# Optimization experiments

Hardware: AMD Instinct MI355X
Metric: run time of the kernel (lower is better)

Reference implementation:

```python
import jax, jax.numpy as jnp
import numpy as np
from jax import lax

# dims
B, N, K = 8, 1024, 32          # batch, nodes, kNN neighbors
D, H, DH = 256, 8, 32           # node feature width, heads, head dim
TDIM, NB, HID = 16, 32, 128     # time-embed dim, radial basis count, radial MLP hidden
NLAYERS = 3                     # hidden transformer layers
L = NLAYERS + 1                 # + output layer
NS = 128                        # scalar channels sliced into edge attrs
SHD = 9                         # spherical harmonics dim for lmax=2 (1+3+5)
RMAX = 2.0
EIN = NB + TDIM + 2 * NS        # edge-MLP input width


def _sph(u):
    # real spherical harmonics l=0,1,2 with 'component' normalization of unit vec u
    x, y, z = u[..., 0], u[..., 1], u[..., 2]
    l0 = jnp.ones_like(x)[..., None]
    l1 = np.sqrt(3.0) * u
    l2 = jnp.stack([
        np.sqrt(15.0) * x * y,
        np.sqrt(15.0) * y * z,
        0.5 * np.sqrt(5.0) * (3.0 * z * z - 1.0),
        np.sqrt(15.0) * x * z,
        0.5 * np.sqrt(15.0) * (x * x - y * y),
    ], -1)
    return jnp.concatenate([l0, l1, l2], -1)


def _rbf(r):
    # e3nn soft_one_hot_linspace(basis='gaussian', cutoff=False) * sqrt(NB) * 0.95
    centers = jnp.linspace(0.0, RMAX, NB)
    step = RMAX / (NB - 1)
    e = jnp.exp(-((r[..., None] - centers) / step) ** 2) / 1.12
    return e * (NB ** 0.5) * 0.95


def _sus(x):
    # e3nn smooth unit step: exp(-1/x) for x>0 else 0
    return jnp.where(x > 0, jnp.exp(-1.0 / jnp.where(x > 0, x, 1.0)), 0.0)


def setup_inputs() -> dict:
    key = jax.random.key(0)
    ks = jax.random.split(key, 12)
    g = lambda k, shape, fan: (jax.random.normal(k, shape, jnp.float32) / np.sqrt(fan))
    return {
        'x': jax.random.normal(ks[0], (B, N, 3), jnp.float32),
        'y': jax.random.normal(ks[1], (B, N, 3), jnp.float32),
        't': jax.random.uniform(ks[2], (B, TDIM), jnp.float32),
        'W_embed': g(ks[3], (3 + TDIM, D), 3 + TDIM),
        'Wk1': g(ks[4], (L, EIN, HID), EIN),
        'bk1': jnp.zeros((L, HID), jnp.float32),
        'Wk2': g(ks[5], (L, HID, H * DH), HID),
        'Wq': g(ks[6], (L, D, H * DH), D),
        'Wv': g(ks[7], (L, D + SHD, H * DH), D + SHD),
        'Wo': g(ks[8], (NLAYERS, H * DH, D), H * DH),
        'Wo_out': g(ks[9], (H * DH, 3), H * DH),
    }


def _forward(x, y, t, W_embed, Wk1, bk1, Wk2, Wq, Wv, Wo, Wo_out):
    def score(pos, feat, tt):
        # kNN graph: full pairwise distance + top_k (self included, as in source)
        d2 = jnp.sum((pos[:, None, :] - pos[None, :, :]) ** 2, -1)      # [N,N]
        src = lax.top_k(-d2, K)[1]                                       # [N,K], dst = row index
        vec = pos[:, None, :] - pos[src]                                 # pos[dst]-pos[src], [N,K,3]
        r = jnp.linalg.norm(vec, axis=-1)                                # [N,K]
        u = vec / jnp.maximum(r[..., None], 1e-9)
        sh = _sph(u)                                                     # [N,K,SHD]
        cut = 1.4 * _sus(10.0 * (1.0 - r / RMAX))                        # [N,K]
        rbf = _rbf(r) * cut[..., None]                                   # [N,K,NB]
        t_nodes = jnp.broadcast_to(tt, (N, TDIM))
        edge_base = jnp.concatenate([rbf, jnp.broadcast_to(tt, (N, K, TDIM))], -1)
        node = jnp.concatenate([feat, t_nodes], -1) @ W_embed            # [N,D]
        for l in range(L):
            # gather scalar node channels onto edges
            e = jnp.concatenate([edge_base, node[src][..., :NS],
                                 jnp.broadcast_to(node[:, None, :NS], (N, K, NS))], -1)  # [N,K,EIN]
            h = jax.nn.gelu(e @ Wk1[l] + bk1[l])                          # radial MLP
            kf = (h @ Wk2[l]).reshape(N, K, H, DH)
            q = (node @ Wq[l]).reshape(N, H, DH)
            logits = jnp.einsum('nhd,nkhd->nkh', q, kf) / np.sqrt(DH)
            # cutoff-weighted softmax over neighbors (e3nn Transformer style)
            w = cut[..., None] * jnp.exp(logits - logits.max(1, keepdims=True))
            alpha = w / (w.sum(1, keepdims=True) + 1e-9)                  # [N,K,H]
            v = (jnp.concatenate([node[src], sh], -1) @ Wv[l]).reshape(N, K, H, DH)
            agg = jnp.einsum('nkh,nkhd->nhd', alpha, v).reshape(N, H * DH)
            if l < NLAYERS:
                node = node + agg @ Wo[l]                                  # residual
                # scalar activation: gelu on 0e, tanh on 0o, identity on higher l
                node = jnp.concatenate([jax.nn.gelu(node[:, :64]),
                                        jnp.tanh(node[:, 64:NS]),
                                        node[:, NS:]], -1)
            else:
                node = agg @ Wo_out                                        # project to 1x1e
        return node  # [N,3]

    return jax.vmap(score)(x, y, t)


def reference(x, y, t, W_embed, Wk1, bk1, Wk2, Wq, Wv, Wo, Wo_out):
    return _forward(x, y, t, W_embed, Wk1, bk1, Wk2, Wq, Wv, Wo, Wo_out)
```

## Files before the change

kernel.cpp:

```cpp
#include <hip/hip_runtime.h>
#include <math.h>

#define Bb 8
#define Nn 1024
#define Kk 32
#define Dd 256
#define Hh 8
#define DHh 32
#define TDIMt 16
#define NBnb 32
#define HIDh 128
#define NSns 128
#define SHDs 9
#define EINe 304
#define NCOLS 1536

typedef __bf16 bf16_t;
typedef bf16_t bf16x8 __attribute__((ext_vector_type(8)));
typedef float floatx4 __attribute__((ext_vector_type(4)));

#define GLOAD_LDS16(gp, lp) __builtin_amdgcn_global_load_lds( \
    (const __attribute__((address_space(1))) void*)(gp),      \
    (__attribute__((address_space(3))) void*)(lp), 16, 0, 0)

__device__ __forceinline__ float gelu_fast(float x){
  float g = 1.5957691216057308f*(x + 0.044715f*x*x*x);
  return x*__builtin_amdgcn_rcpf(1.0f + __expf(-g));
}
__device__ __forceinline__ float tanh_fast(float x){
  return 1.0f - 2.0f*__builtin_amdgcn_rcpf(1.0f + __expf(2.0f*x));
}

__global__ __launch_bounds__(256) void setup_kernel(
    const float* __restrict__ x, const float* __restrict__ y, const float* __restrict__ t,
    const float* __restrict__ We, const float* __restrict__ Wk1, const float* __restrict__ bk1,
    const float* __restrict__ Wk2, const float* __restrict__ Wq, const float* __restrict__ Wv,
    const float* __restrict__ Wo,
    bf16_t* __restrict__ Wt, bf16_t* __restrict__ Wto, bf16_t* __restrict__ WrbfT,
    float* __restrict__ t_hd, int* __restrict__ src,
    float* __restrict__ node, bf16_t* __restrict__ node_bf){

  __shared__ float s_b[32];
  __shared__ unsigned long long s_knn[4][64];
  const int bid = blockIdx.x, tid = threadIdx.x;

  if (bid < 2048){
    int wave = tid >> 6, lane = tid & 63;
    int bn = bid*4 + wave;
    int b = bn >> 10, n = bn & (Nn-1);
    const float* xb = x + (size_t)b*Nn*3;
    float px = xb[n*3+0], py = xb[n*3+1], pz = xb[n*3+2];
    float d2v[16];
    #pragma unroll
    for (int i=0;i<16;i++){
      int j = i*64 + lane;
      float dx = px - xb[j*3+0];
      float dy = py - xb[j*3+1];
      float dz = pz - xb[j*3+2];
      d2v[i] = dx*dx + dy*dy + dz*dz;
    }

    unsigned lob = 0u, hib = 0x7149F2CAu;
    float T = 1.0f;
    int lc = 0;
    for (int it=0; it<24; ++it){
      lc = 0;
      #pragma unroll
      for (int i=0;i<16;i++) lc += (d2v[i] <= T) ? 1 : 0;
      int c = lc;
      #pragma unroll
      for (int off=32; off>=1; off>>=1) c += __shfl_xor(c, off);
      if (c >= 32 && c <= 64) break;
      if (c < 32) lob = __float_as_uint(T); else hib = __float_as_uint(T);
      float ratio = 44.0f * __builtin_amdgcn_rcpf((float)(c < 1 ? 1 : c));
      float Tn = T * __powf(ratio, 0.6666667f);
      unsigned tb = __float_as_uint(Tn);
      if (tb <= lob || tb >= hib) tb = lob + ((hib - lob) >> 1);
      T = __uint_as_float(tb);
    }

    int pre = lc;
    #pragma unroll
    for (int d=1; d<64; d<<=1){
      int o = __shfl_up(pre, d);
      if (lane >= d) pre += o;
    }
    int wo = pre - lc;

    unsigned long long* sl = s_knn[wave];
    sl[lane] = ~0ull;
    #pragma unroll
    for (int i=0;i<16;i++){
      if (d2v[i] <= T && wo < 64){
        sl[wo] = (((unsigned long long)__float_as_uint(d2v[i])) << 10)
                 | (unsigned)(i*64 + lane);
        wo++;
      }
    }
    __syncthreads();

    unsigned long long key = sl[lane];
    #pragma unroll
    for (int k2=2; k2<=64; k2<<=1){
      #pragma unroll
      for (int j2=k2>>1; j2>=1; j2>>=1){
        unsigned long long pv = __shfl_xor(key, j2);
        bool takeMin = (((lane & j2) == 0) == ((lane & k2) == 0));
        bool pLess = pv < key;
        key = (pLess == takeMin) ? pv : key;
      }
    }
    if (lane < 32) src[(size_t)bn*Kk + lane] = (int)(key & 1023u);
  } else if (bid < 6144){
    int i = bid-2048; int l = i>>10, yy = i&1023;
    int h = yy>>7, c = yy&127;
    if (tid < 32) s_b[tid] = Wk2[(size_t)l*HIDh*Dd + (size_t)c*Dd + h*DHh + tid];
    __syncthreads();
    const int rloc = tid>>3, dg = tid&7;
    const float b0 = s_b[dg*4+0], b1 = s_b[dg*4+1], b2 = s_b[dg*4+2], b3 = s_b[dg*4+3];
    #pragma unroll
    for (int p=0;p<8;p++){
      int ii = p*32 + rloc;
      const float4 v = *(const float4*)(Wq + (size_t)l*Dd*Dd + (size_t)ii*Dd + h*DHh + dg*4);
      float part = v.x*b0 + v.y*b1 + v.z*b2 + v.w*b3;
      part += __shfl_xor(part, 1);
      part += __shfl_xor(part, 2);
      part += __shfl_xor(part, 4);
      if (dg == 0) Wt[((size_t)l*NCOLS + 512 + yy)*Dd + ii] = (bf16_t)part;
    }
  } else if (bid < 8192){
    int i = bid-6144; int l = i>>9, c = i&511, k = tid;
    const float* wk1l = Wk1 + (size_t)l*EINe*HIDh;
    float v;
    if (c < 256)       v = Wv[(size_t)l*265*Dd + (size_t)k*Dd + c];
    else if (c < 384){ int c2 = c-256; v = (k < 128) ? wk1l[(48+k)*HIDh + c2] : 0.0f; }
    else             { int c2 = c-384; v = (k < 128) ? wk1l[(176+k)*HIDh + c2] : 0.0f; }
    Wt[((size_t)l*NCOLS + c)*Dd + k] = (bf16_t)v;
  } else if (bid < 8960){
    int i = bid-8192; int l = i>>8; int c = i&255; int k = tid;
    Wto[((size_t)l*Dd + c)*Dd + k] = (bf16_t)Wo[(size_t)l*Dd*Dd + (size_t)k*Dd + c];
  } else if (bid < 9024){
    int i = bid-8960; int l = i>>4, cg = i&15;
    int c = cg*8 + (tid>>5), k = tid&31;
    WrbfT[((size_t)l*HIDh + c)*NBnb + k] = (bf16_t)Wk1[(size_t)l*EINe*HIDh + (size_t)k*HIDh + c];
  } else if (bid < 9040){
    int i = bid-9024; int pair = i*2 + (tid>>7);
    int l = pair>>3, b = pair&7, c = tid&127;
    const float* wk1l = Wk1 + (size_t)l*EINe*HIDh;
    float a = bk1[l*HIDh + c];
    #pragma unroll
    for (int ii=0;ii<TDIMt;ii++) a += t[b*TDIMt+ii]*wk1l[(32+ii)*HIDh + c];
    t_hd[(l*Bb + b)*HIDh + c] = a;
  } else {
    int bn0 = (bid-9040)*4; int c = tid;
    float w0 = We[0*Dd+c], w1 = We[1*Dd+c], w2 = We[2*Dd+c];
    float wt[TDIMt];
    #pragma unroll
    for (int i=0;i<TDIMt;i++) wt[i] = We[(3+i)*Dd+c];
    #pragma unroll
    for (int u=0;u<4;u++){
      int bn = bn0 + u; int b = bn >> 10;
      float a = y[(size_t)bn*3+0]*w0 + y[(size_t)bn*3+1]*w1 + y[(size_t)bn*3+2]*w2;
      #pragma unroll
      for (int i=0;i<TDIMt;i++) a += t[b*TDIMt+i]*wt[i];
      node[(size_t)bn*Dd + c] = a;
      node_bf[(size_t)bn*Dd + c] = (bf16_t)a;
    }
  }
}

__global__ __launch_bounds__(256) void gemm_proj(const bf16_t* __restrict__ A,
    const bf16_t* __restrict__ Wt_all, float* __restrict__ vproj_f,
    bf16_t* __restrict__ hsrc_bf, float* __restrict__ hdst_f,
    bf16_t* __restrict__ qw_bf, const float* __restrict__ t_hd, int layer){

  __shared__ __align__(16) bf16_t s_A[2][8192];
  __shared__ __align__(16) bf16_t s_B[2][4096];

  const int tid = threadIdx.x;
  const int wave = tid>>6, lane = tid&63;
  const int row16 = lane&15, quad = lane>>4;
  const int bx = blockIdx.x;
  const int brow = ((bx & 7) << 3) + (bx >> 3);
  const int m0 = brow*128;
  const int m_base = m0 + wave*32;
  const int n_base = blockIdx.y*64;
  const bf16_t* Ab = A + (size_t)m0*Dd;
  const bf16_t* Bw = Wt_all + ((size_t)layer*NCOLS + n_base)*Dd;

  const int trow = tid>>3;
  const int tk   = ((tid&7) ^ (trow&7)) << 3;
  const int swz  = (row16&7) << 3;

  floatx4 acc[2][4];
  #pragma unroll
  for (int mi=0;mi<2;mi++)
    #pragma unroll
    for (int ni=0;ni<4;ni++){ floatx4 z = {0.f,0.f,0.f,0.f}; acc[mi][ni] = z; }

  {
    const bf16_t* ga = Ab + (size_t)trow*Dd + tk;
    #pragma unroll
    for (int i=0;i<4;i++) GLOAD_LDS16(ga + (size_t)i*32*Dd, &s_A[0][i*2048 + tid*8]);
    const bf16_t* gb = Bw + (size_t)trow*Dd + tk;
    #pragma unroll
    for (int j=0;j<2;j++) GLOAD_LDS16(gb + (size_t)j*32*Dd, &s_B[0][j*2048 + tid*8]);
  }
  __syncthreads();

  #pragma unroll
  for (int kt=0; kt<4; kt++){
    const int cur = kt&1, nxt = cur^1;
    if (kt < 3){
      const bf16_t* ga = Ab + (size_t)trow*Dd + (kt+1)*64 + tk;
      #pragma unroll
      for (int i=0;i<4;i++) GLOAD_LDS16(ga + (size_t)i*32*Dd, &s_A[nxt][i*2048 + tid*8]);
      const bf16_t* gb = Bw + (size_t)trow*Dd + (kt+1)*64 + tk;
      #pragma unroll
      for (int j=0;j<2;j++) GLOAD_LDS16(gb + (size_t)j*32*Dd, &s_B[nxt][j*2048 + tid*8]);
    }
    #pragma unroll
    for (int ksub=0; ksub<2; ksub++){
      const int ko = (ksub*32 + quad*8) ^ swz;
      bf16x8 a0 = *(const bf16x8*)&s_A[cur][(wave*32      + row16)*64 + ko];
      bf16x8 a1 = *(const bf16x8*)&s_A[cur][(wave*32 + 16 + row16)*64 + ko];
      #pragma unroll
      for (int ni=0;ni<4;ni++){
        bf16x8 b = *(const bf16x8*)&s_B[cur][(ni*16 + row16)*64 + ko];
        acc[0][ni] = __builtin_amdgcn_mfma_f32_16x16x32_bf16(a0, b, acc[0][ni], 0,0,0);
        acc[1][ni] = __builtin_amdgcn_mfma_f32_16x16x32_bf16(a1, b, acc[1][ni], 0,0,0);
      }
    }
    __syncthreads();
  }

  const int by = blockIdx.y;
  const int bb = m_base >> 10;
  #pragma unroll
  for (int mi=0;mi<2;mi++)
    #pragma unroll
    for (int ni=0;ni<4;ni++){
      int col = n_base + ni*16 + row16;
      #pragma unroll
      for (int r=0;r<4;r++){
        int row = m_base + mi*16 + quad*4 + r;
        float v = acc[mi][ni][r];
        if (by < 4)       vproj_f[(size_t)row*256 + col]        = v;
        else if (by < 6)  hsrc_bf[(size_t)row*128 + (col-256)]  = (bf16_t)v;
        else if (by < 8)  hdst_f[(size_t)row*128 + (col-384)]   = v + t_hd[(size_t)(layer*Bb + bb)*HIDh + (col-384)];
        else              qw_bf[(size_t)row*1024 + (col-512)]   = (bf16_t)v;
      }
    }
}

__global__ __launch_bounds__(256) void gemm_upd(
    const bf16_t* __restrict__ agg_bf, const bf16_t* __restrict__ Wto,
    const float* __restrict__ node_in, float* __restrict__ node_out,
    bf16_t* __restrict__ node_bf, int lu, int write_node){

  __shared__ __align__(16) bf16_t s_A[2][8192];
  __shared__ __align__(16) bf16_t s_B[2][4096];

  const int tid = threadIdx.x;
  const int wave = tid>>6, lane = tid&63;
  const int row16 = lane&15, quad = lane>>4;
  const int bx = blockIdx.x;
  const int brow = ((bx & 7) << 3) + (bx >> 3);
  const int m0 = brow*128;
  const int m_base = m0 + wave*32;
  const int n_base = blockIdx.y*64;
  const bf16_t* Ab = agg_bf + (size_t)m0*Dd;
  const bf16_t* Bw = Wto + (size_t)lu*Dd*Dd + (size_t)n_base*Dd;

  const int trow = tid>>3;
  const int tk   = ((tid&7) ^ (trow&7)) << 3;
  const int swz  = (row16&7) << 3;

  floatx4 acc[2][4];
  #pragma unroll
  for (int mi=0;mi<2;mi++)
    #pragma unroll
    for (int ni=0;ni<4;ni++){ floatx4 z = {0.f,0.f,0.f,0.f}; acc[mi][ni] = z; }

  {
    const bf16_t* ga = Ab + (size_t)trow*Dd + tk;
    #pragma unroll
    for (int i=0;i<4;i++) GLOAD_LDS16(ga + (size_t)i*32*Dd, &s_A[0][i*2048 + tid*8]);
    const bf16_t* gb = Bw + (size_t)trow*Dd + tk;
    #pragma unroll
    for (int j=0;j<2;j++) GLOAD_LDS16(gb + (size_t)j*32*Dd, &s_B[0][j*2048 + tid*8]);
  }
  __syncthreads();

  #pragma unroll
  for (int kt=0; kt<4; kt++){
    const int cur = kt&1, nxt = cur^1;
    if (kt < 3){
      const bf16_t* ga = Ab + (size_t)trow*Dd + (kt+1)*64 + tk;
      #pragma unroll
      for (int i=0;i<4;i++) GLOAD_LDS16(ga + (size_t)i*32*Dd, &s_A[nxt][i*2048 + tid*8]);
      const bf16_t* gb = Bw + (size_t)trow*Dd + (kt+1)*64 + tk;
      #pragma unroll
      for (int j=0;j<2;j++) GLOAD_LDS16(gb + (size_t)j*32*Dd, &s_B[nxt][j*2048 + tid*8]);
    }
    #pragma unroll
    for (int ksub=0; ksub<2; ksub++){
      const int ko = (ksub*32 + quad*8) ^ swz;
      bf16x8 a0 = *(const bf16x8*)&s_A[cur][(wave*32      + row16)*64 + ko];
      bf16x8 a1 = *(const bf16x8*)&s_A[cur][(wave*32 + 16 + row16)*64 + ko];
      #pragma unroll
      for (int ni=0;ni<4;ni++){
        bf16x8 b = *(const bf16x8*)&s_B[cur][(ni*16 + row16)*64 + ko];
        acc[0][ni] = __builtin_amdgcn_mfma_f32_16x16x32_bf16(a0, b, acc[0][ni], 0,0,0);
        acc[1][ni] = __builtin_amdgcn_mfma_f32_16x16x32_bf16(a1, b, acc[1][ni], 0,0,0);
      }
    }
    __syncthreads();
  }

  #pragma unroll
  for (int mi=0;mi<2;mi++)
    #pragma unroll
    for (int ni=0;ni<4;ni++){
      int col = n_base + ni*16 + row16;
      #pragma unroll
      for (int r=0;r<4;r++){
        int row = m_base + mi*16 + quad*4 + r;
        float v = acc[mi][ni][r] + node_in[(size_t)row*Dd + col];
        if (col < 64)       v = gelu_fast(v);
        else if (col < 128) v = tanh_fast(v);
        if (write_node) node_out[(size_t)row*Dd + col] = v;
        node_bf[(size_t)row*Dd + col] = (bf16_t)v;
      }
    }
}

__global__ __launch_bounds__(256) void attn_kernel(
    const float* __restrict__ x, const int* __restrict__ src,
    const float* __restrict__ vproj_f, const bf16_t* __restrict__ hsrc_bf,
    const float* __restrict__ hdst_f, const bf16_t* __restrict__ qw_bf,
    const bf16_t* __restrict__ WrbfT,
    const float* __restrict__ Wvg, const float* __restrict__ Woo,
    bf16_t* __restrict__ agg_bf, float* __restrict__ out, int layer){

  __shared__ __align__(16) char smem[23296];
  bf16_t* s_h     = (bf16_t*)(smem);
  float*  s_part  = (float*)(smem);
  float*  s_sh    = (float*)(smem + 17408);
  float*  s_cut   = (float*)(smem + 19968);
  int*    s_srcv  = (int*)  (smem + 20224);
  float*  s_logit = (float*)(smem + 20480);
  float*  s_pool  = (float*)(smem + 22528);
  float*  s_red   = (float*)(smem + 23168);

  const int tid  = threadIdx.x;
  const int bidx = blockIdx.x;
  const int b    = bidx & 7;
  const int bn0  = (b << 10) | ((bidx >> 3) << 1);
  const int wave = tid>>6, lane = tid&63;
  const int side = wave>>1, wv = wave&1;
  const int row16 = lane&15, quad = lane>>4;
  const int bns = bn0 + side;

  bf16x8 qf[4];
  { const bf16_t* qp = qw_bf + (size_t)bns*1024 + row16*HIDh + quad*8;
    #pragma unroll
    for (int ks=0; ks<4; ks++) qf[ks] = *(const bf16x8*)(qp + ks*32); }
  float hdv[4];
  #pragma unroll
  for (int ni=0; ni<4; ni++) hdv[ni] = hdst_f[(size_t)bns*128 + wv*64 + ni*16 + row16];

  const float ax = x[(size_t)bns*3+0], ay = x[(size_t)bns*3+1], az = x[(size_t)bns*3+2];

  const int sE0 = src[(size_t)bns*Kk + row16];
  const int sE1 = src[(size_t)bns*Kk + row16 + 16];

  const int t2 = tid & 127;
  const int e0 = t2>>3, cg = t2&7;
  const int sG0 = src[(size_t)bns*Kk + e0];
  const int sG1 = src[(size_t)bns*Kk + e0 + 16];
  bf16x8 hsv00 = *(const bf16x8*)(hsrc_bf + ((size_t)b*Nn + sG0)*128 + cg*8);
  bf16x8 hsv01 = *(const bf16x8*)(hsrc_bf + ((size_t)b*Nn + sG0)*128 + cg*8 + 64);
  bf16x8 hsv10 = *(const bf16x8*)(hsrc_bf + ((size_t)b*Nn + sG1)*128 + cg*8);
  bf16x8 hsv11 = *(const bf16x8*)(hsrc_bf + ((size_t)b*Nn + sG1)*128 + cg*8 + 64);

  bf16x8 a0f, a1f;
  {
    const float* xj0 = x + ((size_t)b*Nn + sE0)*3;
    const float* xj1 = x + ((size_t)b*Nn + sE1)*3;
    float d0x = ax - xj0[0], d0y = ay - xj0[1], d0z = az - xj0[2];
    float d1x = ax - xj1[0], d1y = ay - xj1[1], d1z = az - xj1[2];
    float rr0 = sqrtf(d0x*d0x + d0y*d0y + d0z*d0z);
    float rr1 = sqrtf(d1x*d1x + d1y*d1y + d1z*d1z);
    float xx0 = 10.0f*(1.0f - rr0*0.5f);
    float xx1 = 10.0f*(1.0f - rr1*0.5f);
    float cu0 = (xx0 > 0.0f) ? 1.4f*__expf(-__builtin_amdgcn_rcpf(xx0)) : 0.0f;
    float cu1 = (xx1 > 0.0f) ? 1.4f*__expf(-__builtin_amdgcn_rcpf(xx1)) : 0.0f;
    float sc0 = 4.798224586623f*cu0;
    float sc1 = 4.798224586623f*cu1;
    float rs0 = fminf(rr0*15.5f, 33.0f);
    float rs1 = fminf(rr1*15.5f, 33.0f);
    float cbase = (float)(quad*8);
    float dd0 = rs0 - cbase, dd1 = rs1 - cbase;
    float e0v = __expf(-dd0*dd0)*sc0;
    float e1v = __expf(-dd1*dd1)*sc1;
    float g0 = __expf(2.0f*dd0 - 1.0f);
    float g1 = __expf(2.0f*dd1 - 1.0f);
    a0f[0] = (bf16_t)e0v; a1f[0] = (bf16_t)e1v;
    #pragma unroll
    for (int j=1;j<8;j++){
      e0v *= g0; e1v *= g1;
      a0f[j] = (bf16_t)e0v; a1f[j] = (bf16_t)e1v;
      g0 *= 0.13533528323661270f; g1 *= 0.13533528323661270f;
    }
  }

  if (tid < 128){
    const int hs = (tid>>6)&1;
    const int k = tid & 31;
    const int hn = bn0 + hs;
    const int j = src[(size_t)hn*Kk + k];
    const float hx = x[(size_t)hn*3+0], hy = x[(size_t)hn*3+1], hz = x[(size_t)hn*3+2];
    const float* xj = x + ((size_t)b*Nn + j)*3;
    float dx = hx - xj[0], dy = hy - xj[1], dz = hz - xj[2];
    float rr = sqrtf(dx*dx + dy*dy + dz*dz);
    if ((tid & 32) == 0){
      s_srcv[hs*32 + k] = j;
      float xx = 10.0f*(1.0f - rr*0.5f);
      s_cut[hs*32 + k] = (xx > 0.0f) ? 1.4f*__expf(-__builtin_amdgcn_rcpf(xx)) : 0.0f;
    } else {
      float inv = __builtin_amdgcn_rcpf(fmaxf(rr, 1e-9f));
      float ux = dx*inv, uy = dy*inv, uz = dz*inv;
      float* sh = s_sh + hs*320 + k*10;
      sh[0] = 1.0f;
      sh[1] = 1.7320508075688772f*ux;
      sh[2] = 1.7320508075688772f*uy;
      sh[3] = 1.7320508075688772f*uz;
      sh[4] = 3.872983346207417f*ux*uy;
      sh[5] = 3.872983346207417f*uy*uz;
      sh[6] = 1.118033988749895f*(3.0f*uz*uz - 1.0f);
      sh[7] = 3.872983346207417f*ux*uz;
      sh[8] = 1.9364916731037085f*(ux*ux - uy*uy);
    }
  }

  floatx4 acc[2][4];
  {
    #pragma unroll
    for (int mi=0;mi<2;mi++)
      #pragma unroll
      for (int ni=0;ni<4;ni++){ floatx4 z = {0.f,0.f,0.f,0.f}; acc[mi][ni] = z; }
    const bf16_t* bp = WrbfT + ((size_t)layer*HIDh + wv*64 + row16)*NBnb + quad*8;
    #pragma unroll
    for (int j=0;j<4;j++){
      bf16x8 bbf = *(const bf16x8*)(bp + (size_t)j*16*NBnb);
      acc[0][j] = __builtin_amdgcn_mfma_f32_16x16x32_bf16(a0f, bbf, acc[0][j], 0,0,0);
      acc[1][j] = __builtin_amdgcn_mfma_f32_16x16x32_bf16(a1f, bbf, acc[1][j], 0,0,0);
    }
  }

  bf16_t* shs = s_h + side*4352;
  *(bf16x8*)(shs + e0*136 + cg*8)            = hsv00;
  *(bf16x8*)(shs + e0*136 + cg*8 + 64)       = hsv01;
  *(bf16x8*)(shs + (e0+16)*136 + cg*8)       = hsv10;
  *(bf16x8*)(shs + (e0+16)*136 + cg*8 + 64)  = hsv11;
  __syncthreads();

  #pragma unroll
  for (int ni=0;ni<4;ni++){
    int c = wv*64 + ni*16 + row16;
    #pragma unroll
    for (int mi=0;mi<2;mi++){
      #pragma unroll
      for (int r=0;r<4;r++){
        int e = mi*16 + quad*4 + r;
        float hs = (float)shs[e*136 + c];
        shs[e*136 + c] = (bf16_t)gelu_fast(acc[mi][ni][r] + hdv[ni] + hs);
      }
    }
  }
  __syncthreads();

  {
    floatx4 la = {0.f,0.f,0.f,0.f};
    #pragma unroll
    for (int ks=0; ks<4; ks++){
      bf16x8 a = *(const bf16x8*)(shs + (wv*16 + row16)*136 + ks*32 + quad*8);
      la = __builtin_amdgcn_mfma_f32_16x16x32_bf16(a, qf[ks], la, 0,0,0);
    }
    if (row16 < Hh){
      #pragma unroll
      for (int r=0;r<4;r++)
        s_logit[side*256 + (wv*16 + quad*4 + r)*8 + row16] = la[r]*0.17677669529663687f;
    }
  }
  __syncthreads();

  {
    const int k = tid & 31;
    const int h = tid >> 5;
    #pragma unroll
    for (int sn=0; sn<2; sn++){
      float lv = s_logit[sn*256 + k*8 + h];
      float m = lv;
      #pragma unroll
      for (int off=16; off>=1; off>>=1) m = fmaxf(m, __shfl_xor(m, off));
      float w = s_cut[sn*32 + k]*__expf(lv - m);
      float ss = w;
      #pragma unroll
      for (int off=16; off>=1; off>>=1) ss += __shfl_xor(ss, off);
      s_logit[sn*256 + k*8 + h] = w*__builtin_amdgcn_rcpf(ss + 1e-9f);
    }
  }
  __syncthreads();

  {
    const int pn = tid>>7, t3 = tid&127, h2 = t3>>4, sg = t3&15;
    if (sg < SHDs){
      float a = 0.0f;
      #pragma unroll
      for (int k2=0;k2<Kk;k2++)
        a += s_logit[pn*256 + k2*8 + h2] * s_sh[pn*320 + k2*10 + sg];
      s_pool[pn*80 + h2*10 + sg] = a;
    }
  }

  {
    const float* rowp[16];
    #pragma unroll
    for (int i=0;i<16;i++){
      int row = __builtin_amdgcn_readfirstlane(s_srcv[side*32 + wv*16 + i]);
      rowp[i] = vproj_f + ((size_t)b*Nn + row)*256;
    }
    const int albase = side*256 + wv*128 + (lane>>3);
    float4 accv = {0.f,0.f,0.f,0.f};
    #pragma unroll
    for (int i=0;i<16;i++){
      const float4 v = *(const float4*)(rowp[i] + (lane<<2));
      float al = s_logit[albase + i*8];
      accv.x += al*v.x; accv.y += al*v.y; accv.z += al*v.z; accv.w += al*v.w;
    }
    *(float4*)(s_part + (side*2 + wv)*256 + (lane<<2)) = accv;
  }
  __syncthreads();

  {
    const int h = tid >> 5;
    const float* wvsh = Wvg + (size_t)layer*265*Dd + 256*Dd;
    float wv9[SHDs];
    #pragma unroll
    for (int sg=0; sg<SHDs; sg++) wv9[sg] = wvsh[sg*Dd + tid];

    float w0=0.f, w1=0.f, w2=0.f;
    if (layer >= 3){ w0 = Woo[tid*3+0]; w1 = Woo[tid*3+1]; w2 = Woo[tid*3+2]; }

    #pragma unroll
    for (int sn=0; sn<2; sn++){
      float a_main = s_part[sn*512 + tid] + s_part[sn*512 + 256 + tid];
      #pragma unroll
      for (int sg=0; sg<SHDs; sg++) a_main += s_pool[sn*80 + h*10 + sg]*wv9[sg];

      if (layer < 3){
        agg_bf[(size_t)(bn0+sn)*Dd + tid] = (bf16_t)a_main;
      } else {
        float p0 = a_main*w0;
        float p1 = a_main*w1;
        float p2 = a_main*w2;
        #pragma unroll
        for (int off=32; off>=1; off>>=1){
          p0 += __shfl_xor(p0, off);
          p1 += __shfl_xor(p1, off);
          p2 += __shfl_xor(p2, off);
        }
        if (lane == 0){
          s_red[sn*12 + wave*3+0] = p0;
          s_red[sn*12 + wave*3+1] = p1;
          s_red[sn*12 + wave*3+2] = p2;
        }
      }
    }
    if (layer >= 3){
      __syncthreads();
      if (tid < 8){
        int sn = tid>>2, j = tid&3;
        if (j < 3)
          out[(size_t)(bn0+sn)*3 + j] = s_red[sn*12 + j] + s_red[sn*12 + 3 + j]
                                      + s_red[sn*12 + 6 + j] + s_red[sn*12 + 9 + j];
      }
    }
  }
}

extern "C" void kernel_launch(void* const* d_in, const int* in_sizes, int n_in,
                              void* d_out, int out_size, void* d_ws, size_t ws_size,
                              hipStream_t stream){
  const float* x   = (const float*)d_in[0];
  const float* y   = (const float*)d_in[1];
  const float* t   = (const float*)d_in[2];
  const float* We  = (const float*)d_in[3];
  const float* Wk1 = (const float*)d_in[4];
  const float* bk1 = (const float*)d_in[5];
  const float* Wk2 = (const float*)d_in[6];
  const float* Wq  = (const float*)d_in[7];
  const float* Wv  = (const float*)d_in[8];
  const float* Wo  = (const float*)d_in[9];
  const float* Woo = (const float*)d_in[10];
  float* out = (float*)d_out;

  char* ws = (char*)d_ws;
  size_t off = 0;
  auto take = [&](size_t bytes)->char*{ char* p = ws + off; off = (off + bytes + 255) & ~(size_t)255; return p; };

  int*    src      = (int*)   take((size_t)Bb*Nn*Kk*4);
  float*  nodeA    = (float*) take((size_t)Bb*Nn*Dd*4);
  float*  nodeB    = (float*) take((size_t)Bb*Nn*Dd*4);
  bf16_t* node_bf  = (bf16_t*)take((size_t)Bb*Nn*Dd*2);
  bf16_t* agg_bf   = (bf16_t*)take((size_t)Bb*Nn*Dd*2);
  float*  vproj_f  = (float*) take((size_t)Bb*Nn*256*4);
  bf16_t* hsrc_bf  = (bf16_t*)take((size_t)Bb*Nn*128*2);
  float*  hdst_f   = (float*) take((size_t)Bb*Nn*128*4);
  bf16_t* qw_bf    = (bf16_t*)take(((size_t)Bb*Nn*1024 + 2048)*2);
  bf16_t* Wt       = (bf16_t*)take((size_t)4*NCOLS*Dd*2);
  bf16_t* Wto      = (bf16_t*)take((size_t)3*Dd*Dd*2);
  bf16_t* WrbfT    = (bf16_t*)take((size_t)4*HIDh*NBnb*2);
  float*  t_hd     = (float*) take((size_t)4*Bb*HIDh*4);

  setup_kernel<<<dim3(11088), 256, 0, stream>>>(x, y, t, We, Wk1, bk1, Wk2, Wq, Wv, Wo,
                                                Wt, Wto, WrbfT, t_hd, src, nodeA, node_bf);

  gemm_proj<<<dim3(64,24), 256, 0, stream>>>(node_bf, Wt, vproj_f, hsrc_bf, hdst_f, qw_bf, t_hd, 0);
  attn_kernel<<<dim3(Bb*Nn/2), 256, 0, stream>>>(x, src, vproj_f, hsrc_bf, hdst_f, qw_bf,
                                                 WrbfT, Wv, Woo, agg_bf, out, 0);
  const float* nin[3]  = {nodeA, nodeB, nodeA};
  float*       nout[3] = {nodeB, nodeA, nodeB};
  for (int l=1; l<4; l++){
    gemm_upd<<<dim3(64,4), 256, 0, stream>>>(agg_bf, Wto, nin[l-1], nout[l-1], node_bf,
                                             l-1, (l < 3) ? 1 : 0);
    gemm_proj<<<dim3(64,24), 256, 0, stream>>>(node_bf, Wt, vproj_f, hsrc_bf, hdst_f, qw_bf, t_hd, l);
    attn_kernel<<<dim3(Bb*Nn/2), 256, 0, stream>>>(x, src, vproj_f, hsrc_bf, hdst_f, qw_bf,
                                                   WrbfT, Wv, Woo, agg_bf, out, l);
  }
}
```

Measured before the change: 391.4 us.

## Process one node per 128-thread attention block instead of two per 256-thread block

Result: no change. 399.0 us (+1.9%).

```diff
diff --git a/kernel.cpp b/kernel.cpp
--- a/kernel.cpp
+++ b/kernel.cpp
@@ -335,7 +335,7 @@
     }
 }
 
-__global__ __launch_bounds__(256) void attn_kernel(
+__global__ __launch_bounds__(128) void attn_kernel(
     const float* __restrict__ x, const int* __restrict__ src,
     const float* __restrict__ vproj_f, const bf16_t* __restrict__ hsrc_bf,
     const float* __restrict__ hdst_f, const bf16_t* __restrict__ qw_bf,
@@ -343,42 +343,38 @@
     const float* __restrict__ Wvg, const float* __restrict__ Woo,
     bf16_t* __restrict__ agg_bf, float* __restrict__ out, int layer){
 
-  __shared__ __align__(16) char smem[23296];
+  __shared__ __align__(16) char smem[11488];
   bf16_t* s_h     = (bf16_t*)(smem);
   float*  s_part  = (float*)(smem);
-  float*  s_sh    = (float*)(smem + 17408);
-  float*  s_cut   = (float*)(smem + 19968);
-  int*    s_srcv  = (int*)  (smem + 20224);
-  float*  s_logit = (float*)(smem + 20480);
-  float*  s_pool  = (float*)(smem + 22528);
-  float*  s_red   = (float*)(smem + 23168);
+  float*  s_sh    = (float*)(smem + 8704);
+  float*  s_cut   = (float*)(smem + 9984);
+  float*  s_logit = (float*)(smem + 10112);
+  float*  s_pool  = (float*)(smem + 11136);
+  float*  s_red   = (float*)(smem + 11456);
 
   const int tid  = threadIdx.x;
   const int bidx = blockIdx.x;
   const int b    = bidx & 7;
-  const int bn0  = (b << 10) | ((bidx >> 3) << 1);
-  const int wave = tid>>6, lane = tid&63;
-  const int side = wave>>1, wv = wave&1;
+  const int bn   = (b << 10) | (bidx >> 3);
+  const int wv   = tid>>6, lane = tid&63;
   const int row16 = lane&15, quad = lane>>4;
-  const int bns = bn0 + side;
 
   bf16x8 qf[4];
-  { const bf16_t* qp = qw_bf + (size_t)bns*1024 + row16*HIDh + quad*8;
+  { const bf16_t* qp = qw_bf + (size_t)bn*1024 + row16*HIDh + quad*8;
     #pragma unroll
     for (int ks=0; ks<4; ks++) qf[ks] = *(const bf16x8*)(qp + ks*32); }
   float hdv[4];
   #pragma unroll
-  for (int ni=0; ni<4; ni++) hdv[ni] = hdst_f[(size_t)bns*128 + wv*64 + ni*16 + row16];
-
-  const float ax = x[(size_t)bns*3+0], ay = x[(size_t)bns*3+1], az = x[(size_t)bns*3+2];
-
-  const int sE0 = src[(size_t)bns*Kk + row16];
-  const int sE1 = src[(size_t)bns*Kk + row16 + 16];
-
-  const int t2 = tid & 127;
-  const int e0 = t2>>3, cg = t2&7;
-  const int sG0 = src[(size_t)bns*Kk + e0];
-  const int sG1 = src[(size_t)bns*Kk + e0 + 16];
+  for (int ni=0; ni<4; ni++) hdv[ni] = hdst_f[(size_t)bn*128 + wv*64 + ni*16 + row16];
+
+  const float ax = x[(size_t)bn*3+0], ay = x[(size_t)bn*3+1], az = x[(size_t)bn*3+2];
+
+  const int sE0 = src[(size_t)bn*Kk + row16];
+  const int sE1 = src[(size_t)bn*Kk + row16 + 16];
+
+  const int e0 = tid>>3, cg = tid&7;
+  const int sG0 = src[(size_t)bn*Kk + e0];
+  const int sG1 = src[(size_t)bn*Kk + e0 + 16];
   bf16x8 hsv00 = *(const bf16x8*)(hsrc_bf + ((size_t)b*Nn + sG0)*128 + cg*8);
   bf16x8 hsv01 = *(const bf16x8*)(hsrc_bf + ((size_t)b*Nn + sG0)*128 + cg*8 + 64);
   bf16x8 hsv10 = *(const bf16x8*)(hsrc_bf + ((size_t)b*Nn + sG1)*128 + cg*8);
@@ -415,23 +411,19 @@
     }
   }
 
-  if (tid < 128){
-    const int hs = (tid>>6)&1;
+  if (tid < 64){
     const int k = tid & 31;
-    const int hn = bn0 + hs;
-    const int j = src[(size_t)hn*Kk + k];
-    const float hx = x[(size_t)hn*3+0], hy = x[(size_t)hn*3+1], hz = x[(size_t)hn*3+2];
+    const int j = src[(size_t)bn*Kk + k];
     const float* xj = x + ((size_t)b*Nn + j)*3;
-    float dx = hx - xj[0], dy = hy - xj[1], dz = hz - xj[2];
+    float dx = ax - xj[0], dy = ay - xj[1], dz = az - xj[2];
     float rr = sqrtf(dx*dx + dy*dy + dz*dz);
-    if ((tid & 32) == 0){
-      s_srcv[hs*32 + k] = j;
+    if (tid < 32){
       float xx = 10.0f*(1.0f - rr*0.5f);
-      s_cut[hs*32 + k] = (xx > 0.0f) ? 1.4f*__expf(-__builtin_amdgcn_rcpf(xx)) : 0.0f;
+      s_cut[k] = (xx > 0.0f) ? 1.4f*__expf(-__builtin_amdgcn_rcpf(xx)) : 0.0f;
     } else {
       float inv = __builtin_amdgcn_rcpf(fmaxf(rr, 1e-9f));
       float ux = dx*inv, uy = dy*inv, uz = dz*inv;
-      float* sh = s_sh + hs*320 + k*10;
+      float* sh = s_sh + k*10;
       sh[0] = 1.0f;
       sh[1] = 1.7320508075688772f*ux;
       sh[2] = 1.7320508075688772f*uy;
@@ -459,11 +451,10 @@
     }
   }
 
-  bf16_t* shs = s_h + side*4352;
-  *(bf16x8*)(shs + e0*136 + cg*8)            = hsv00;
-  *(bf16x8*)(shs + e0*136 + cg*8 + 64)       = hsv01;
-  *(bf16x8*)(shs + (e0+16)*136 + cg*8)       = hsv10;
-  *(bf16x8*)(shs + (e0+16)*136 + cg*8 + 64)  = hsv11;
+  *(bf16x8*)(s_h + e0*136 + cg*8)            = hsv00;
+  *(bf16x8*)(s_h + e0*136 + cg*8 + 64)       = hsv01;
+  *(bf16x8*)(s_h + (e0+16)*136 + cg*8)       = hsv10;
+  *(bf16x8*)(s_h + (e0+16)*136 + cg*8 + 64)  = hsv11;
   __syncthreads();
 
   #pragma unroll
@@ -474,8 +465,8 @@
       #pragma unroll
       for (int r=0;r<4;r++){
         int e = mi*16 + quad*4 + r;
-        float hs = (float)shs[e*136 + c];
-        shs[e*136 + c] = (bf16_t)gelu_fast(acc[mi][ni][r] + hdv[ni] + hs);
+        float hs = (float)s_h[e*136 + c];
+        s_h[e*136 + c] = (bf16_t)gelu_fast(acc[mi][ni][r] + hdv[ni] + hs);
       }
     }
   }
@@ -485,43 +476,44 @@
     floatx4 la = {0.f,0.f,0.f,0.f};
     #pragma unroll
     for (int ks=0; ks<4; ks++){
-      bf16x8 a = *(const bf16x8*)(shs + (wv*16 + row16)*136 + ks*32 + quad*8);
+      bf16x8 a = *(const bf16x8*)(s_h + (wv*16 + row16)*136 + ks*32 + quad*8);
       la = __builtin_amdgcn_mfma_f32_16x16x32_bf16(a, qf[ks], la, 0,0,0);
     }
     if (row16 < Hh){
       #pragma unroll
       for (int r=0;r<4;r++)
-        s_logit[side*256 + (wv*16 + quad*4 + r)*8 + row16] = la[r]*0.17677669529663687f;
+        s_logit[(wv*16 + quad*4 + r)*8 + row16] = la[r]*0.17677669529663687f;
     }
   }
   __syncthreads();
 
   {
     const int k = tid & 31;
-    const int h = tid >> 5;
-    #pragma unroll
-    for (int sn=0; sn<2; sn++){
-      float lv = s_logit[sn*256 + k*8 + h];
+    const int h0 = tid >> 5;
+    #pragma unroll
+    for (int hh=0; hh<2; hh++){
+      const int h = h0 + hh*4;
+      float lv = s_logit[k*8 + h];
       float m = lv;
       #pragma unroll
       for (int off=16; off>=1; off>>=1) m = fmaxf(m, __shfl_xor(m, off));
-      float w = s_cut[sn*32 + k]*__expf(lv - m);
+      float w = s_cut[k]*__expf(lv - m);
       float ss = w;
       #pragma unroll
       for (int off=16; off>=1; off>>=1) ss += __shfl_xor(ss, off);
-      s_logit[sn*256 + k*8 + h] = w*__builtin_amdgcn_rcpf(ss + 1e-9f);
+      s_logit[k*8 + h] = w*__builtin_amdgcn_rcpf(ss + 1e-9f);
     }
   }
   __syncthreads();
 
   {
-    const int pn = tid>>7, t3 = tid&127, h2 = t3>>4, sg = t3&15;
+    const int h2 = tid>>4, sg = tid&15;
     if (sg < SHDs){
       float a = 0.0f;
       #pragma unroll
       for (int k2=0;k2<Kk;k2++)
-        a += s_logit[pn*256 + k2*8 + h2] * s_sh[pn*320 + k2*10 + sg];
-      s_pool[pn*80 + h2*10 + sg] = a;
+        a += s_logit[k2*8 + h2] * s_sh[k2*10 + sg];
+      s_pool[h2*10 + sg] = a;
     }
   }
 
@@ -529,10 +521,10 @@
     const float* rowp[16];
     #pragma unroll
     for (int i=0;i<16;i++){
-      int row = __builtin_amdgcn_readfirstlane(s_srcv[side*32 + wv*16 + i]);
+      int row = __builtin_amdgcn_readfirstlane(src[(size_t)bn*Kk + wv*16 + i]);
       rowp[i] = vproj_f + ((size_t)b*Nn + row)*256;
     }
-    const int albase = side*256 + wv*128 + (lane>>3);
+    const int albase = wv*128 + (lane>>3);
     float4 accv = {0.f,0.f,0.f,0.f};
     #pragma unroll
     for (int i=0;i<16;i++){
@@ -540,53 +532,40 @@
       float al = s_logit[albase + i*8];
       accv.x += al*v.x; accv.y += al*v.y; accv.z += al*v.z; accv.w += al*v.w;
     }
-    *(float4*)(s_part + (side*2 + wv)*256 + (lane<<2)) = accv;
+    *(float4*)(s_part + wv*256 + (lane<<2)) = accv;
   }
   __syncthreads();
 
   {
-    const int h = tid >> 5;
     const float* wvsh = Wvg + (size_t)layer*265*Dd + 256*Dd;
-    float wv9[SHDs];
-    #pragma unroll
-    for (int sg=0; sg<SHDs; sg++) wv9[sg] = wvsh[sg*Dd + tid];
-
-    float w0=0.f, w1=0.f, w2=0.f;
-    if (layer >= 3){ w0 = Woo[tid*3+0]; w1 = Woo[tid*3+1]; w2 = Woo[tid*3+2]; }
-
-    #pragma unroll
-    for (int sn=0; sn<2; sn++){
-      float a_main = s_part[sn*512 + tid] + s_part[sn*512 + 256 + tid];
-      #pragma unroll
-      for (int sg=0; sg<SHDs; sg++) a_main += s_pool[sn*80 + h*10 + sg]*wv9[sg];
+    float p0 = 0.f, p1 = 0.f, p2 = 0.f;
+    #pragma unroll
+    for (int cc=0; cc<2; cc++){
+      const int c = tid + cc*128;
+      const int h = c >> 5;
+      float a_main = s_part[c] + s_part[256 + c];
+      #pragma unroll
+      for (int sg=0; sg<SHDs; sg++) a_main += s_pool[h*10 + sg]*wvsh[sg*Dd + c];
 
       if (layer < 3){
-        agg_bf[(size_t)(bn0+sn)*Dd + tid] = (bf16_t)a_main;
+        agg_bf[(size_t)bn*Dd + c] = (bf16_t)a_main;
       } else {
-        float p0 = a_main*w0;
-        float p1 = a_main*w1;
-        float p2 = a_main*w2;
-        #pragma unroll
-        for (int off=32; off>=1; off>>=1){
-          p0 += __shfl_xor(p0, off);
-          p1 += __shfl_xor(p1, off);
-          p2 += __shfl_xor(p2, off);
-        }
-        if (lane == 0){
-          s_red[sn*12 + wave*3+0] = p0;
-          s_red[sn*12 + wave*3+1] = p1;
-          s_red[sn*12 + wave*3+2] = p2;
-        }
+        p0 += a_main*Woo[c*3+0];
+        p1 += a_main*Woo[c*3+1];
+        p2 += a_main*Woo[c*3+2];
       }
     }
     if (layer >= 3){
+      #pragma unroll
+      for (int off=32; off>=1; off>>=1){
+        p0 += __shfl_xor(p0, off);
+        p1 += __shfl_xor(p1, off);
+        p2 += __shfl_xor(p2, off);
+      }
+      if (lane == 0){ s_red[wv*3+0]=p0; s_red[wv*3+1]=p1; s_red[wv*3+2]=p2; }
       __syncthreads();
-      if (tid < 8){
-        int sn = tid>>2, j = tid&3;
-        if (j < 3)
-          out[(size_t)(bn0+sn)*3 + j] = s_red[sn*12 + j] + s_red[sn*12 + 3 + j]
-                                      + s_red[sn*12 + 6 + j] + s_red[sn*12 + 9 + j];
-      }
+      if (tid < 3)
+        out[(size_t)bn*3 + tid] = s_red[tid] + s_red[3+tid];
     }
   }
 }
@@ -629,15 +608,15 @@
                                                 Wt, Wto, WrbfT, t_hd, src, nodeA, node_bf);
 
   gemm_proj<<<dim3(64,24), 256, 0, stream>>>(node_bf, Wt, vproj_f, hsrc_bf, hdst_f, qw_bf, t_hd, 0);
-  attn_kernel<<<dim3(Bb*Nn/2), 256, 0, stream>>>(x, src, vproj_f, hsrc_bf, hdst_f, qw_bf,
-                                                 WrbfT, Wv, Woo, agg_bf, out, 0);
+  attn_kernel<<<dim3(Bb*Nn), 128, 0, stream>>>(x, src, vproj_f, hsrc_bf, hdst_f, qw_bf,
+                                               WrbfT, Wv, Woo, agg_bf, out, 0);
   const float* nin[3]  = {nodeA, nodeB, nodeA};
   float*       nout[3] = {nodeB, nodeA, nodeB};
   for (int l=1; l<4; l++){
     gemm_upd<<<dim3(64,4), 256, 0, stream>>>(agg_bf, Wto, nin[l-1], nout[l-1], node_bf,
                                              l-1, (l < 3) ? 1 : 0);
     gemm_proj<<<dim3(64,24), 256, 0, stream>>>(node_bf, Wt, vproj_f, hsrc_bf, hdst_f, qw_bf, t_hd, l);
-    attn_kernel<<<dim3(Bb*Nn/2), 256, 0, stream>>>(x, src, vproj_f, hsrc_bf, hdst_f, qw_bf,
-                                                   WrbfT, Wv, Woo, agg_bf, out, l);
+    attn_kernel<<<dim3(Bb*Nn), 128, 0, stream>>>(x, src, vproj_f, hsrc_bf, hdst_f, qw_bf,
+                                                 WrbfT, Wv, Woo, agg_bf, out, l);
   }
 }
```
